# Performance work log

Measured on AMD Instinct MI355X. Metric: run time of the kernel, lower is better.

The kernel has to match this reference:

```python
import jax, jax.numpy as jnp
import numpy as np

N = 100000   # entities
T = 4        # edge types
E = 250000   # edges per type
D = 64       # dimension
H = 4        # attention heads
C = 64       # per-head out channels (PyG out_channels)
F_IN = 256   # raw feature dim
L = 2        # num_layers
NEG_SLOPE = 0.2


def setup_inputs() -> dict:
    key = jax.random.key(0)
    ks = jax.random.split(key, 10)
    return {
        "feature_matrix": jax.random.normal(ks[0], (N, F_IN), jnp.float32),
        "entity_emb": jax.random.normal(ks[1], (N + 1, D), jnp.float32),
        "lin_w": jax.random.normal(ks[2], (F_IN, D), jnp.float32) * 0.05,
        "lin_b": jnp.zeros((D,), jnp.float32),
        "ln_g": jnp.ones((D,), jnp.float32),
        "ln_b": jnp.zeros((D,), jnp.float32),
        "W_src": jax.random.normal(ks[3], (L, T, D, H * C), jnp.float32) * 0.1,
        "W_dst": jax.random.normal(ks[4], (L, T, D, H * C), jnp.float32) * 0.1,
        "a_src": jax.random.normal(ks[5], (L, T, H, C), jnp.float32) * 0.1,
        "a_dst": jax.random.normal(ks[6], (L, T, H, C), jnp.float32) * 0.1,
        "conv_bias": jnp.zeros((L, T, C), jnp.float32),
        "edge_index": jax.random.randint(ks[7], (T, 2, E), 0, N, jnp.int32),
    }


def _layer_norm(x, g, b):
    mu = jnp.mean(x, axis=-1, keepdims=True)
    var = jnp.var(x, axis=-1, keepdims=True)
    return (x - mu) * jax.lax.rsqrt(var + 1e-5) * g + b


def _l2_normalize(x):
    n = jnp.linalg.norm(x, axis=-1, keepdims=True)
    return x / jnp.maximum(n, 1e-12)


def _gat_conv(x, src, dst, Ws, Wd, a_s, a_d, bias):
    # x: [N, D]; src/dst: [E'] (self loops already appended, PyG default)
    xs = (x @ Ws).reshape(N, H, C)          # source projection per head
    xd = (x @ Wd).reshape(N, H, C)          # destination projection per head
    logit = (xs * a_s).sum(-1)[src] + (xd * a_d).sum(-1)[dst]  # [E', H]
    logit = jax.nn.leaky_relu(logit, NEG_SLOPE)
    # segment softmax over incoming edges of each dst node
    m = jax.lax.stop_gradient(jax.ops.segment_max(logit, dst, num_segments=N))
    p = jnp.exp(logit - m[dst])
    s = jax.ops.segment_sum(p, dst, num_segments=N)
    alpha = p / s[dst]                       # [E', H]
    msg = xs[src] * alpha[..., None]         # [E', H, C]
    out = jax.ops.segment_sum(msg.reshape(-1, H * C), dst, num_segments=N)
    out = out.reshape(N, H, C).mean(axis=1)  # concat=False -> head mean
    return out + bias


def reference(feature_matrix, entity_emb, lin_w, lin_b, ln_g, ln_b,
              W_src, W_dst, a_src, a_dst, conv_bias, edge_index):
    # feature_transform: Linear -> LayerNorm -> GELU (exact erf GELU, torch default)
    xf = jax.nn.gelu(_layer_norm(feature_matrix @ lin_w + lin_b, ln_g, ln_b),
                     approximate=False)
    xe = _l2_normalize(entity_emb[:N])
    x = xf + xe
    loop = jnp.arange(N, dtype=edge_index.dtype)
    for l in range(L):
        acc = jnp.zeros((N, C), x.dtype)
        for t in range(T):
            src = jnp.concatenate([edge_index[t, 0], loop])
            dst = jnp.concatenate([edge_index[t, 1], loop])
            acc = acc + _gat_conv(x, src, dst, W_src[l, t], W_dst[l, t],
                                  a_src[l, t], a_dst[l, t], conv_bias[l, t])
        x = jax.nn.gelu(acc / T, approximate=False)  # HeteroConv aggr='mean'; dropout=eval identity
    return x
```

## Files before the change

### kernel.cpp

```cpp
#include <hip/hip_runtime.h>
#include <hip/hip_bf16.h>
#include <cstdint>

#define NN   100000
#define TT   4
#define EE   250000
#define LL   2
#define NCH  49
#define EPN  (EE + NN)
#define N64  ((size_t)NN * 64)

typedef unsigned short ushort_t;
typedef __attribute__((ext_vector_type(8))) short bf16x8;
typedef __attribute__((ext_vector_type(16))) float floatx16;

static __device__ __forceinline__ float gelu_exact(float v) {
    return 0.5f * v * (1.0f + erff(v * 0.7071067811865476f));
}
static __device__ __forceinline__ float wave_sum64(float v) {
    #pragma unroll
    for (int m = 32; m; m >>= 1) v += __shfl_xor(v, m, 64);
    return v;
}
static __device__ __forceinline__ ushort_t f2bf(float f) {
    unsigned u = __float_as_uint(f);
    u += 0x7FFFu + ((u >> 16) & 1u);
    return (ushort_t)(u >> 16);
}
static __device__ __forceinline__ float bf2f(ushort_t h) {
    return __uint_as_float((unsigned)h << 16);
}
static __device__ __forceinline__ void gl_lds16(const ushort_t* g, ushort_t* l) {
    __builtin_amdgcn_global_load_lds(
        (const __attribute__((address_space(1))) void*)g,
        (__attribute__((address_space(3))) void*)l, 16, 0, 0);
}

__global__ __launch_bounds__(256) void k_prep(
    const float* __restrict__ Wsrc, const float* __restrict__ Wdst,
    const float* __restrict__ asrc, const float* __restrict__ adst,
    const float* __restrict__ cb, const float* __restrict__ lin_w,
    ushort_t* __restrict__ wcTh, ushort_t* __restrict__ wcTl,
    ushort_t* __restrict__ lwTh, ushort_t* __restrict__ lwTl,
    ushort_t* __restrict__ bpTh, ushort_t* __restrict__ bpTl,
    float* __restrict__ bsum)
{
    int id = blockIdx.x * 256 + threadIdx.x;
    {
        int d = id & 63;
        int c = (id >> 6) & 63;
        int h = (id >> 12) & 3;
        int t = (id >> 14) & 3;
        int l = (id >> 16) & 1;
        float v = 0.25f * Wsrc[(((l * 4 + t) * 64 + d) * 256) + h * 64 + c];
        int dst = (l * 64 + c) * 1024 + (t * 256 + h * 64 + d);
        ushort_t hh = f2bf(v);
        bpTh[dst] = hh;
        bpTl[dst] = f2bf(v - bf2f(hh));
    }
    if (id < LL * 64 * 64) {
        int d   = id & 63;
        int col = (id >> 6) & 63;
        int l   = (id >> 12) & 1;
        int t = col >> 3, side = (col >> 2) & 1, h = col & 3;
        const float* W = side ? Wdst : Wsrc;
        const float* a = side ? adst : asrc;
        int wb = ((l * 4 + t) * 64 + d) * 256 + h * 64;
        int ab = ((l * 4 + t) * 4 + h) * 64;
        float s = 0.f;
        #pragma unroll 8
        for (int c2 = 0; c2 < 64; ++c2) s = fmaf(W[wb + c2], a[ab + c2], s);
        int dst = (l * 64 + col) * 64 + d;
        ushort_t hh = f2bf(s);
        wcTh[dst] = hh;
        wcTl[dst] = f2bf(s - bf2f(hh));
    }
    if (id < 64 * 256) {
        int k = id & 255, c = id >> 8;
        float v = lin_w[k * 64 + c];
        ushort_t hh = f2bf(v);
        lwTh[c * 256 + k] = hh;
        lwTl[c * 256 + k] = f2bf(v - bf2f(hh));
    }
    if (id < LL * 64) {
        int l = id >> 6, c = id & 63;
        float s = 0.f;
        for (int t = 0; t < TT; ++t) s += cb[(l * 4 + t) * 64 + c];
        bsum[id] = s;
    }
}

__global__ void k_hist(const int* __restrict__ ei, int* __restrict__ cursor) {
    int id = blockIdx.x * 256 + threadIdx.x;
    if (id >= TT * EE) return;
    int t = id / EE, e = id - t * EE;
    int d = ei[(t * 2 + 1) * EE + e];
    atomicAdd(&cursor[t * NN + d], 1);
}

__global__ __launch_bounds__(256) void k_scan1(const int* __restrict__ deg,
                                               int* __restrict__ csum) {
    int b = blockIdx.x, t = b / NCH, cc = b - t * NCH;
    int tid = threadIdx.x;
    int base = cc * 2048 + tid * 8;
    int s = 0;
    #pragma unroll
    for (int i = 0; i < 8; ++i) {
        int idx = base + i;
        if (idx < NN) s += deg[t * NN + idx] + 1;
    }
    #pragma unroll
    for (int m = 32; m; m >>= 1) s += __shfl_xor(s, m, 64);
    __shared__ int ws4[4];
    int lane = tid & 63, wid = tid >> 6;
    if (lane == 0) ws4[wid] = s;
    __syncthreads();
    if (tid == 0) csum[b] = ws4[0] + ws4[1] + ws4[2] + ws4[3];
}

__global__ void k_scan2(const int* __restrict__ csum, int* __restrict__ cbase,
                        int* __restrict__ row_ptr) {
    int t = threadIdx.x;
    if (t >= TT) return;
    int base = 0;
    for (int c = 0; c < NCH; ++c) {
        cbase[t * NCH + c] = base;
        base += csum[t * NCH + c];
    }
    row_ptr[t * (NN + 1) + NN] = base;
}

__global__ __launch_bounds__(256) void k_scan3(int* __restrict__ cursor,
                                               const int* __restrict__ cbase,
                                               int* __restrict__ row_ptr) {
    int b = blockIdx.x, t = b / NCH, cc = b - t * NCH;
    int tid = threadIdx.x, lane = tid & 63, wid = tid >> 6;
    int base = cc * 2048 + tid * 8;
    int vals[8], ts = 0;
    #pragma unroll
    for (int i = 0; i < 8; ++i) {
        int idx = base + i;
        int v = (idx < NN) ? cursor[t * NN + idx] + 1 : 0;
        vals[i] = v; ts += v;
    }
    int v = ts;
    #pragma unroll
    for (int off = 1; off < 64; off <<= 1) {
        int u = __shfl_up(v, off, 64);
        if (lane >= off) v += u;
    }
    __shared__ int wt[4];
    if (lane == 63) wt[wid] = v;
    __syncthreads();
    int wbase = 0;
    for (int w = 0; w < wid; ++w) wbase += wt[w];
    int run = cbase[t * NCH + cc] + wbase + (v - ts);
    #pragma unroll
    for (int i = 0; i < 8; ++i) {
        int idx = base + i;
        if (idx < NN) {
            row_ptr[t * (NN + 1) + idx] = run;
            cursor[t * NN + idx] = run;
        }
        run += vals[i];
    }
}

__global__ void k_scatter(const int* __restrict__ ei, int* __restrict__ cursor,
                          int2* __restrict__ sd) {
    int id = blockIdx.x * 256 + threadIdx.x;
    if (id >= TT * EPN) return;
    int t = id / EPN, r = id - t * EPN;
    int s, d;
    if (r < EE) { s = ei[t * 2 * EE + r]; d = ei[(t * 2 + 1) * EE + r]; }
    else        { s = d = r - EE; }
    int pos = atomicAdd(&cursor[t * NN + d], 1);
    sd[(size_t)t * EPN + pos] = make_int2(s, d);
}

template <int FLAGS>
__global__ __launch_bounds__(256, 4) void k_gemm_mx(
    const ushort_t* __restrict__ Ahi, const ushort_t* __restrict__ Alo,
    const ushort_t* __restrict__ Bhi, const ushort_t* __restrict__ Blo,
    int K, int ldb, int nrows,
    const float* __restrict__ accbuf, const float* __restrict__ bias,
    float* __restrict__ Cout)
{
    constexpr int KC = 32;
    __shared__ ushort_t sAh[128 * 32], sAl[128 * 32];
    __shared__ ushort_t sBh[64 * 32],  sBl[64 * 32];
    const int tid = threadIdx.x;
    const int w = tid >> 6, ln = tid & 63;
    const int l31 = ln & 31, hl = ln >> 5;
    const int rowbase = blockIdx.x * 128;

    floatx16 accv[2];
    #pragma unroll
    for (int ct = 0; ct < 2; ++ct)
        #pragma unroll
        for (int r = 0; r < 16; ++r) accv[ct][r] = 0.f;

    for (int kc = 0; kc < K; kc += KC) {
        __syncthreads();
        #pragma unroll
        for (int i = 0; i < 2; ++i) {
            int f = tid + i * 256;
            int r = f >> 2, cg = f & 3;
            int row = rowbase + r;
            int sg = (r ^ (r >> 2)) & 3;
            if constexpr (FLAGS & 8) {
                int sw = r * 32 + ((cg ^ sg) << 3);
                if (row < nrows) {
                    const float* Af = (const float*)Ahi;
                    size_t ga = (size_t)row * K + kc + cg * 8;
                    float4 v0 = *(const float4*)(Af + ga);
                    float4 v1 = *(const float4*)(Af + ga + 4);
                    float vf[8] = {v0.x, v0.y, v0.z, v0.w, v1.x, v1.y, v1.z, v1.w};
                    unsigned hu[8], lu[8];
                    #pragma unroll
                    for (int q = 0; q < 8; ++q) {
                        ushort_t hh = f2bf(vf[q]);
                        hu[q] = hh;
                        lu[q] = f2bf(vf[q] - bf2f(hh));
                    }
                    uint4 H = make_uint4(hu[0] | (hu[1] << 16), hu[2] | (hu[3] << 16),
                                         hu[4] | (hu[5] << 16), hu[6] | (hu[7] << 16));
                    uint4 L = make_uint4(lu[0] | (lu[1] << 16), lu[2] | (lu[3] << 16),
                                         lu[4] | (lu[5] << 16), lu[6] | (lu[7] << 16));
                    *(uint4*)&sAh[sw] = H;
                    *(uint4*)&sAl[sw] = L;
                } else {
                    *(uint4*)&sAh[sw] = make_uint4(0, 0, 0, 0);
                    *(uint4*)&sAl[sw] = make_uint4(0, 0, 0, 0);
                }
            } else {
                int so = r * 32 + (cg << 3);
                size_t ga = (size_t)row * K + kc + ((cg ^ sg) << 3);
                if (row < nrows) {
                    gl_lds16(Ahi + ga, &sAh[so]);
                    gl_lds16(Alo + ga, &sAl[so]);
                }
            }
        }
        {
            int r = tid >> 2, cg = tid & 3;
            int sg = (r ^ (r >> 2)) & 3;
            int so = r * 32 + (cg << 3);
            size_t gb = (size_t)r * ldb + kc + ((cg ^ sg) << 3);
            gl_lds16(Bhi + gb, &sBh[so]);
            gl_lds16(Blo + gb, &sBl[so]);
        }
        __syncthreads();
        const int arow = (w << 5) + l31;
        const int sga = (arow ^ (arow >> 2)) & 3;
        const int sgb = (l31 ^ (l31 >> 2)) & 3;
        #pragma unroll
        for (int s = 0; s < 2; ++s) {
            const int c0 = (s << 1) | hl;
            const int ka = (c0 ^ sga) << 3;
            const int kb = (c0 ^ sgb) << 3;
            bf16x8 ah  = *(const bf16x8*)&sAh[arow * 32 + ka];
            bf16x8 al  = *(const bf16x8*)&sAl[arow * 32 + ka];
            bf16x8 bh0 = *(const bf16x8*)&sBh[l31 * 32 + kb];
            bf16x8 bl0 = *(const bf16x8*)&sBl[l31 * 32 + kb];
            bf16x8 bh1 = *(const bf16x8*)&sBh[(32 + l31) * 32 + kb];
            bf16x8 bl1 = *(const bf16x8*)&sBl[(32 + l31) * 32 + kb];
            accv[0] = __builtin_amdgcn_mfma_f32_32x32x16_bf16(ah, bh0, accv[0], 0, 0, 0);
            accv[1] = __builtin_amdgcn_mfma_f32_32x32x16_bf16(ah, bh1, accv[1], 0, 0, 0);
            accv[0] = __builtin_amdgcn_mfma_f32_32x32x16_bf16(al, bh0, accv[0], 0, 0, 0);
            accv[1] = __builtin_amdgcn_mfma_f32_32x32x16_bf16(al, bh1, accv[1], 0, 0, 0);
            accv[0] = __builtin_amdgcn_mfma_f32_32x32x16_bf16(ah, bl0, accv[0], 0, 0, 0);
            accv[1] = __builtin_amdgcn_mfma_f32_32x32x16_bf16(ah, bl1, accv[1], 0, 0, 0);
        }
    }
    #pragma unroll
    for (int ct = 0; ct < 2; ++ct) {
        int col = (ct << 5) + l31;
        float bv = (FLAGS & 2) ? bias[col] : 0.f;
        #pragma unroll
        for (int r = 0; r < 16; ++r) {
            int row = rowbase + (w << 5) + (r & 3) + ((r >> 2) << 3) + (hl << 2);
            if (row < nrows) {
                size_t idx = (size_t)row * 64 + col;
                float v = accv[ct][r];
                if (FLAGS & 1) v += accbuf[idx];
                if (FLAGS & 2) v = gelu_exact((v + bv) * 0.25f);
                Cout[idx] = v;
            }
        }
    }
}

__global__ __launch_bounds__(256) void k_feat_post(
    const float* __restrict__ y, const float* __restrict__ lin_b,
    const float* __restrict__ ln_g, const float* __restrict__ ln_b,
    const float* __restrict__ emb, float* __restrict__ xout)
{
    int n = (blockIdx.x << 2) + (threadIdx.x >> 6);
    int c = threadIdx.x & 63;
    size_t base = (size_t)n * 64 + c;
    float v = y[base] + lin_b[c];
    float mean = wave_sum64(v) * 0.015625f;
    float t = v - mean;
    float var = wave_sum64(t * t) * 0.015625f;
    float vn = t * (1.0f / sqrtf(var + 1e-5f)) * ln_g[c] + ln_b[c];
    float g = gelu_exact(vn);
    float e = emb[base];
    float nrm = sqrtf(wave_sum64(e * e));
    float xv = g + e / fmaxf(nrm, 1e-12f);
    xout[base] = xv;
}

__global__ __launch_bounds__(256) void k_edgep(
    const float* __restrict__ s_all, const int2* __restrict__ sd,
    float* __restrict__ parr)
{
    int i = blockIdx.x * 256 + threadIdx.x;
    int t = blockIdx.y;
    if (i >= EPN) return;
    size_t base = (size_t)t * EPN + i;
    int2 e = sd[base];
    const float4 a = *(const float4*)&s_all[(size_t)e.x * 64 + t * 8];
    const float4 b = *(const float4*)&s_all[(size_t)e.y * 64 + t * 8 + 4];
    float l0 = a.x + b.x, l1 = a.y + b.y;
    float l2 = a.z + b.z, l3 = a.w + b.w;
    l0 = l0 > 0.f ? l0 : 0.2f * l0;
    l1 = l1 > 0.f ? l1 : 0.2f * l1;
    l2 = l2 > 0.f ? l2 : 0.2f * l2;
    l3 = l3 > 0.f ? l3 : 0.2f * l3;
    float4 p = make_float4(__expf(l0), __expf(l1), __expf(l2), __expf(l3));
    *(float4*)&parr[base * 4] = p;
}

__global__ __launch_bounds__(256) void k_edge2(
    const float* __restrict__ x, const float* __restrict__ parr,
    const int* __restrict__ row_ptr, const int2* __restrict__ sd,
    ushort_t* __restrict__ zh, ushort_t* __restrict__ zl, int t0)
{
    int n = (blockIdx.x << 2) + (threadIdx.x >> 6);
    int lane = threadIdx.x & 63;
    const int tA = t0, tB = t0 + 1;
    int eA  = row_ptr[tA * (NN + 1) + n];
    int eA1 = row_ptr[tA * (NN + 1) + n + 1];
    int eB  = row_ptr[tB * (NN + 1) + n];
    int eB1 = row_ptr[tB * (NN + 1) + n + 1];
    const int2*   sdA = sd + (size_t)tA * EPN;
    const float4* pA  = (const float4*)parr + (size_t)tA * EPN;
    const int2*   sdB = sd + (size_t)tB * EPN;
    const float4* pB  = (const float4*)parr + (size_t)tB * EPN;
    float a0 = 0.f, a1 = 0.f, a2 = 0.f, a3 = 0.f;
    float SA0 = 0.f, SA1 = 0.f, SA2 = 0.f, SA3 = 0.f;
    float b0 = 0.f, b1 = 0.f, b2 = 0.f, b3 = 0.f;
    float SB0 = 0.f, SB1 = 0.f, SB2 = 0.f, SB3 = 0.f;
    int m = (eA1 - eA < eB1 - eB) ? (eA1 - eA) : (eB1 - eB);
    #pragma unroll 2
    for (int i = 0; i < m; ++i) {
        int sA_ = sdA[eA + i].x;
        int sB_ = sdB[eB + i].x;
        float4 pa = pA[eA + i];
        float4 pb = pB[eB + i];
        float xa = x[(size_t)sA_ * 64 + lane];
        float xb = x[(size_t)sB_ * 64 + lane];
        SA0 += pa.x; SA1 += pa.y; SA2 += pa.z; SA3 += pa.w;
        SB0 += pb.x; SB1 += pb.y; SB2 += pb.z; SB3 += pb.w;
        a0 = fmaf(pa.x, xa, a0); a1 = fmaf(pa.y, xa, a1);
        a2 = fmaf(pa.z, xa, a2); a3 = fmaf(pa.w, xa, a3);
        b0 = fmaf(pb.x, xb, b0); b1 = fmaf(pb.y, xb, b1);
        b2 = fmaf(pb.z, xb, b2); b3 = fmaf(pb.w, xb, b3);
    }
    eA += m; eB += m;
    for (; eA < eA1; ++eA) {
        int s = sdA[eA].x; float4 p = pA[eA];
        float xv = x[(size_t)s * 64 + lane];
        SA0 += p.x; SA1 += p.y; SA2 += p.z; SA3 += p.w;
        a0 = fmaf(p.x, xv, a0); a1 = fmaf(p.y, xv, a1);
        a2 = fmaf(p.z, xv, a2); a3 = fmaf(p.w, xv, a3);
    }
    for (; eB < eB1; ++eB) {
        int s = sdB[eB].x; float4 p = pB[eB];
        float xv = x[(size_t)s * 64 + lane];
        SB0 += p.x; SB1 += p.y; SB2 += p.z; SB3 += p.w;
        b0 = fmaf(p.x, xv, b0); b1 = fmaf(p.y, xv, b1);
        b2 = fmaf(p.z, xv, b2); b3 = fmaf(p.w, xv, b3);
    }
    size_t zb = (size_t)n * 512 + lane;
    {
        float v0 = a0 / SA0, v1 = a1 / SA1, v2 = a2 / SA2, v3 = a3 / SA3;
        ushort_t h0 = f2bf(v0), h1 = f2bf(v1), h2 = f2bf(v2), h3 = f2bf(v3);
        zh[zb]       = h0;  zl[zb]       = f2bf(v0 - bf2f(h0));
        zh[zb + 64]  = h1;  zl[zb + 64]  = f2bf(v1 - bf2f(h1));
        zh[zb + 128] = h2;  zl[zb + 128] = f2bf(v2 - bf2f(h2));
        zh[zb + 192] = h3;  zl[zb + 192] = f2bf(v3 - bf2f(h3));
    }
    {
        size_t zc = zb + 256;
        float v0 = b0 / SB0, v1 = b1 / SB1, v2 = b2 / SB2, v3 = b3 / SB3;
        ushort_t h0 = f2bf(v0), h1 = f2bf(v1), h2 = f2bf(v2), h3 = f2bf(v3);
        zh[zc]       = h0;  zl[zc]       = f2bf(v0 - bf2f(h0));
        zh[zc + 64]  = h1;  zl[zc + 64]  = f2bf(v1 - bf2f(h1));
        zh[zc + 128] = h2;  zl[zc + 128] = f2bf(v2 - bf2f(h2));
        zh[zc + 192] = h3;  zl[zc + 192] = f2bf(v3 - bf2f(h3));
    }
}

extern "C" void kernel_launch(void* const* d_in, const int* in_sizes, int n_in,
                              void* d_out, int out_size, void* d_ws, size_t ws_size,
                              hipStream_t stream) {
    const float* fm    = (const float*)d_in[0];
    const float* emb   = (const float*)d_in[1];
    const float* lin_w = (const float*)d_in[2];
    const float* lin_b = (const float*)d_in[3];
    const float* ln_g  = (const float*)d_in[4];
    const float* ln_b  = (const float*)d_in[5];
    const float* Wsrc  = (const float*)d_in[6];
    const float* Wdst  = (const float*)d_in[7];
    const float* asrc  = (const float*)d_in[8];
    const float* adst  = (const float*)d_in[9];
    const float* cbias = (const float*)d_in[10];
    const int*   ei    = (const int*)d_in[11];
    float* out = (float*)d_out;
    (void)in_sizes; (void)n_in; (void)out_size; (void)ws_size;

    char* w = (char*)d_ws;
    size_t off = 0;
    auto alloc = [&](size_t bytes) -> void* {
        void* p = w + off;
        off += (bytes + 255) & ~(size_t)255;
        return p;
    };
    ushort_t* wcTh = (ushort_t*)alloc((size_t)LL * 64 * 64 * 2);
    ushort_t* wcTl = (ushort_t*)alloc((size_t)LL * 64 * 64 * 2);
    ushort_t* lwTh = (ushort_t*)alloc((size_t)64 * 256 * 2);
    ushort_t* lwTl = (ushort_t*)alloc((size_t)64 * 256 * 2);
    ushort_t* bpTh = (ushort_t*)alloc((size_t)LL * 64 * 1024 * 2);
    ushort_t* bpTl = (ushort_t*)alloc((size_t)LL * 64 * 1024 * 2);
    float* bsum    = (float*)alloc((size_t)LL * 64 * 4);
    int*   row_ptr = (int*)  alloc((size_t)TT * (NN + 1) * 4);
    int*   cursor  = (int*)  alloc((size_t)TT * NN * 4);
    int2*  sdarr   = (int2*) alloc((size_t)TT * EPN * 8);
    float* parr    = (float*)alloc((size_t)TT * EPN * 4 * 4);
    int*   csum    = (int*)  alloc((size_t)TT * NCH * 4);
    int*   cbase   = (int*)  alloc((size_t)TT * NCH * 4);
    float* x       = (float*)alloc(N64 * 4);
    float* s_all   = (float*)alloc(N64 * 4);
    float* accB    = (float*)alloc(N64 * 4);
    size_t planeE = (size_t)NN * 512;
    ushort_t* zh = (ushort_t*)alloc(2 * planeE * 2);
    ushort_t* zl = zh + planeE;

    hipMemsetAsync(cursor, 0, (size_t)TT * NN * 4, stream);
    k_prep<<<512, 256, 0, stream>>>(Wsrc, Wdst, asrc, adst, cbias, lin_w,
                                    wcTh, wcTl, lwTh, lwTl, bpTh, bpTl, bsum);
    k_hist<<<(TT * EE + 255) / 256, 256, 0, stream>>>(ei, cursor);
    k_scan1<<<TT * NCH, 256, 0, stream>>>(cursor, csum);
    k_scan2<<<1, 64, 0, stream>>>(csum, cbase, row_ptr);
    k_scan3<<<TT * NCH, 256, 0, stream>>>(cursor, cbase, row_ptr);
    k_scatter<<<(TT * EPN + 255) / 256, 256, 0, stream>>>(ei, cursor, sdarr);

    const int GB = (NN + 127) / 128;
    k_gemm_mx<8><<<GB, 256, 0, stream>>>((const ushort_t*)fm, nullptr,
                                         lwTh, lwTl, 256, 256, NN,
                                         nullptr, nullptr, accB);
    k_feat_post<<<NN / 4, 256, 0, stream>>>(accB, lin_b, ln_g, ln_b, emb, x);

    const dim3 gp((EPN + 255) / 256, TT);
    for (int l = 0; l < LL; ++l) {
        float* dest = (l == 0) ? x : out;
        k_gemm_mx<8><<<GB, 256, 0, stream>>>((const ushort_t*)x, nullptr,
                                             wcTh + l * 4096, wcTl + l * 4096,
                                             64, 64, NN, nullptr, nullptr, s_all);
        k_edgep<<<gp, 256, 0, stream>>>(s_all, sdarr, parr);
        const ushort_t* Bh = bpTh + (size_t)l * 65536;
        const ushort_t* Bl = bpTl + (size_t)l * 65536;
        k_edge2<<<NN / 4, 256, 0, stream>>>(x, parr, row_ptr, sdarr, zh, zl, 0);
        k_gemm_mx<0><<<GB, 256, 0, stream>>>(zh, zl, Bh, Bl, 512, 1024, NN,
                                             nullptr, nullptr, accB);
        k_edge2<<<NN / 4, 256, 0, stream>>>(x, parr, row_ptr, sdarr, zh, zl, 2);
        k_gemm_mx<3><<<GB, 256, 0, stream>>>(zh, zl, Bh + 512, Bl + 512, 512, 1024,
                                             NN, accB, bsum + l * 64, dest);
    }
}
```

Measured before the change: 1.024 ms.

## Fuse edge aggregation with projection GEMM via shared-memory bf16 staging

Replaces the two edge-aggregation kernels and two split bf16 GEMMs per layer with one fused kernel. Each block aggregates attention-weighted neighbor features for 64 nodes per edge type into LDS as hi/lo bf16, then multiplies by the per-type projection with MFMA, and applies bias plus GELU at the end. This removes the large z intermediate (N×512 hi/lo planes) written to and read back from global memory, and uses ping-pong x buffers. The cost is lower occupancy from about 64KB of LDS per block and serialization between the gather phase and the MFMA phase within a block.

```diff
diff --git a/kernel.cpp b/kernel.cpp
--- a/kernel.cpp
+++ b/kernel.cpp
@@ -13,6 +13,7 @@
 typedef unsigned short ushort_t;
 typedef __attribute__((ext_vector_type(8))) short bf16x8;
 typedef __attribute__((ext_vector_type(16))) float floatx16;
+typedef __attribute__((ext_vector_type(4))) float floatx4;
 
 static __device__ __forceinline__ float gelu_exact(float v) {
     return 0.5f * v * (1.0f + erff(v * 0.7071067811865476f));
@@ -53,7 +54,7 @@
         int t = (id >> 14) & 3;
         int l = (id >> 16) & 1;
         float v = 0.25f * Wsrc[(((l * 4 + t) * 64 + d) * 256) + h * 64 + c];
-        int dst = (l * 64 + c) * 1024 + (t * 256 + h * 64 + d);
+        int dst = (l * 64 + c) * 1024 + (t * 256 + d * 4 + h);
         ushort_t hh = f2bf(v);
         bpTh[dst] = hh;
         bpTl[dst] = f2bf(v - bf2f(hh));
@@ -178,13 +179,10 @@
     sd[(size_t)t * EPN + pos] = make_int2(s, d);
 }
 
-template <int FLAGS>
-__global__ __launch_bounds__(256, 4) void k_gemm_mx(
-    const ushort_t* __restrict__ Ahi, const ushort_t* __restrict__ Alo,
+__global__ __launch_bounds__(256, 4) void k_gemm_f32a(
+    const float* __restrict__ Af,
     const ushort_t* __restrict__ Bhi, const ushort_t* __restrict__ Blo,
-    int K, int ldb, int nrows,
-    const float* __restrict__ accbuf, const float* __restrict__ bias,
-    float* __restrict__ Cout)
+    int K, int ldb, int nrows, float* __restrict__ Cout)
 {
     constexpr int KC = 32;
     __shared__ ushort_t sAh[128 * 32], sAl[128 * 32];
@@ -208,38 +206,28 @@
             int r = f >> 2, cg = f & 3;
             int row = rowbase + r;
             int sg = (r ^ (r >> 2)) & 3;
-            if constexpr (FLAGS & 8) {
-                int sw = r * 32 + ((cg ^ sg) << 3);
-                if (row < nrows) {
-                    const float* Af = (const float*)Ahi;
-                    size_t ga = (size_t)row * K + kc + cg * 8;
-                    float4 v0 = *(const float4*)(Af + ga);
-                    float4 v1 = *(const float4*)(Af + ga + 4);
-                    float vf[8] = {v0.x, v0.y, v0.z, v0.w, v1.x, v1.y, v1.z, v1.w};
-                    unsigned hu[8], lu[8];
-                    #pragma unroll
-                    for (int q = 0; q < 8; ++q) {
-                        ushort_t hh = f2bf(vf[q]);
-                        hu[q] = hh;
-                        lu[q] = f2bf(vf[q] - bf2f(hh));
-                    }
-                    uint4 H = make_uint4(hu[0] | (hu[1] << 16), hu[2] | (hu[3] << 16),
-                                         hu[4] | (hu[5] << 16), hu[6] | (hu[7] << 16));
-                    uint4 L = make_uint4(lu[0] | (lu[1] << 16), lu[2] | (lu[3] << 16),
-                                         lu[4] | (lu[5] << 16), lu[6] | (lu[7] << 16));
-                    *(uint4*)&sAh[sw] = H;
-                    *(uint4*)&sAl[sw] = L;
-                } else {
-                    *(uint4*)&sAh[sw] = make_uint4(0, 0, 0, 0);
-                    *(uint4*)&sAl[sw] = make_uint4(0, 0, 0, 0);
+            int sw = r * 32 + ((cg ^ sg) << 3);
+            if (row < nrows) {
+                size_t ga = (size_t)row * K + kc + cg * 8;
+                floatx4 v0 = *(const floatx4*)(Af + ga);
+                floatx4 v1 = *(const floatx4*)(Af + ga + 4);
+                float vf[8] = {v0.x, v0.y, v0.z, v0.w, v1.x, v1.y, v1.z, v1.w};
+                unsigned hu[8], lu[8];
+                #pragma unroll
+                for (int q = 0; q < 8; ++q) {
+                    ushort_t hh = f2bf(vf[q]);
+                    hu[q] = hh;
+                    lu[q] = f2bf(vf[q] - bf2f(hh));
                 }
+                uint4 H = make_uint4(hu[0] | (hu[1] << 16), hu[2] | (hu[3] << 16),
+                                     hu[4] | (hu[5] << 16), hu[6] | (hu[7] << 16));
+                uint4 L = make_uint4(lu[0] | (lu[1] << 16), lu[2] | (lu[3] << 16),
+                                     lu[4] | (lu[5] << 16), lu[6] | (lu[7] << 16));
+                *(uint4*)&sAh[sw] = H;
+                *(uint4*)&sAl[sw] = L;
             } else {
-                int so = r * 32 + (cg << 3);
-                size_t ga = (size_t)row * K + kc + ((cg ^ sg) << 3);
-                if (row < nrows) {
-                    gl_lds16(Ahi + ga, &sAh[so]);
-                    gl_lds16(Alo + ga, &sAl[so]);
-                }
+                *(uint4*)&sAh[sw] = make_uint4(0, 0, 0, 0);
+                *(uint4*)&sAl[sw] = make_uint4(0, 0, 0, 0);
             }
         }
         {
@@ -276,17 +264,10 @@
     #pragma unroll
     for (int ct = 0; ct < 2; ++ct) {
         int col = (ct << 5) + l31;
-        float bv = (FLAGS & 2) ? bias[col] : 0.f;
         #pragma unroll
         for (int r = 0; r < 16; ++r) {
             int row = rowbase + (w << 5) + (r & 3) + ((r >> 2) << 3) + (hl << 2);
-            if (row < nrows) {
-                size_t idx = (size_t)row * 64 + col;
-                float v = accv[ct][r];
-                if (FLAGS & 1) v += accbuf[idx];
-                if (FLAGS & 2) v = gelu_exact((v + bv) * 0.25f);
-                Cout[idx] = v;
-            }
+            if (row < nrows) Cout[(size_t)row * 64 + col] = accv[ct][r];
         }
     }
 }
@@ -332,74 +313,137 @@
     *(float4*)&parr[base * 4] = p;
 }
 
-__global__ __launch_bounds__(256) void k_edge2(
+__global__ __launch_bounds__(256) void k_fused(
     const float* __restrict__ x, const float* __restrict__ parr,
     const int* __restrict__ row_ptr, const int2* __restrict__ sd,
-    ushort_t* __restrict__ zh, ushort_t* __restrict__ zl, int t0)
+    const ushort_t* __restrict__ Bh, const ushort_t* __restrict__ Bl,
+    const float* __restrict__ bias, float* __restrict__ dest)
 {
-    int n = (blockIdx.x << 2) + (threadIdx.x >> 6);
-    int lane = threadIdx.x & 63;
-    const int tA = t0, tB = t0 + 1;
-    int eA  = row_ptr[tA * (NN + 1) + n];
-    int eA1 = row_ptr[tA * (NN + 1) + n + 1];
-    int eB  = row_ptr[tB * (NN + 1) + n];
-    int eB1 = row_ptr[tB * (NN + 1) + n + 1];
-    const int2*   sdA = sd + (size_t)tA * EPN;
-    const float4* pA  = (const float4*)parr + (size_t)tA * EPN;
-    const int2*   sdB = sd + (size_t)tB * EPN;
-    const float4* pB  = (const float4*)parr + (size_t)tB * EPN;
-    float a0 = 0.f, a1 = 0.f, a2 = 0.f, a3 = 0.f;
-    float SA0 = 0.f, SA1 = 0.f, SA2 = 0.f, SA3 = 0.f;
-    float b0 = 0.f, b1 = 0.f, b2 = 0.f, b3 = 0.f;
-    float SB0 = 0.f, SB1 = 0.f, SB2 = 0.f, SB3 = 0.f;
-    int m = (eA1 - eA < eB1 - eB) ? (eA1 - eA) : (eB1 - eB);
-    #pragma unroll 2
-    for (int i = 0; i < m; ++i) {
-        int sA_ = sdA[eA + i].x;
-        int sB_ = sdB[eB + i].x;
-        float4 pa = pA[eA + i];
-        float4 pb = pB[eB + i];
-        float xa = x[(size_t)sA_ * 64 + lane];
-        float xb = x[(size_t)sB_ * 64 + lane];
-        SA0 += pa.x; SA1 += pa.y; SA2 += pa.z; SA3 += pa.w;
-        SB0 += pb.x; SB1 += pb.y; SB2 += pb.z; SB3 += pb.w;
-        a0 = fmaf(pa.x, xa, a0); a1 = fmaf(pa.y, xa, a1);
-        a2 = fmaf(pa.z, xa, a2); a3 = fmaf(pa.w, xa, a3);
-        b0 = fmaf(pb.x, xb, b0); b1 = fmaf(pb.y, xb, b1);
-        b2 = fmaf(pb.z, xb, b2); b3 = fmaf(pb.w, xb, b3);
-    }
-    eA += m; eB += m;
-    for (; eA < eA1; ++eA) {
-        int s = sdA[eA].x; float4 p = pA[eA];
-        float xv = x[(size_t)s * 64 + lane];
-        SA0 += p.x; SA1 += p.y; SA2 += p.z; SA3 += p.w;
-        a0 = fmaf(p.x, xv, a0); a1 = fmaf(p.y, xv, a1);
-        a2 = fmaf(p.z, xv, a2); a3 = fmaf(p.w, xv, a3);
-    }
-    for (; eB < eB1; ++eB) {
-        int s = sdB[eB].x; float4 p = pB[eB];
-        float xv = x[(size_t)s * 64 + lane];
-        SB0 += p.x; SB1 += p.y; SB2 += p.z; SB3 += p.w;
-        b0 = fmaf(p.x, xv, b0); b1 = fmaf(p.y, xv, b1);
-        b2 = fmaf(p.z, xv, b2); b3 = fmaf(p.w, xv, b3);
-    }
-    size_t zb = (size_t)n * 512 + lane;
-    {
-        float v0 = a0 / SA0, v1 = a1 / SA1, v2 = a2 / SA2, v3 = a3 / SA3;
-        ushort_t h0 = f2bf(v0), h1 = f2bf(v1), h2 = f2bf(v2), h3 = f2bf(v3);
-        zh[zb]       = h0;  zl[zb]       = f2bf(v0 - bf2f(h0));
-        zh[zb + 64]  = h1;  zl[zb + 64]  = f2bf(v1 - bf2f(h1));
-        zh[zb + 128] = h2;  zl[zb + 128] = f2bf(v2 - bf2f(h2));
-        zh[zb + 192] = h3;  zl[zb + 192] = f2bf(v3 - bf2f(h3));
-    }
-    {
-        size_t zc = zb + 256;
-        float v0 = b0 / SB0, v1 = b1 / SB1, v2 = b2 / SB2, v3 = b3 / SB3;
-        ushort_t h0 = f2bf(v0), h1 = f2bf(v1), h2 = f2bf(v2), h3 = f2bf(v3);
-        zh[zc]       = h0;  zl[zc]       = f2bf(v0 - bf2f(h0));
-        zh[zc + 64]  = h1;  zl[zc + 64]  = f2bf(v1 - bf2f(h1));
-        zh[zc + 128] = h2;  zl[zc + 128] = f2bf(v2 - bf2f(h2));
-        zh[zc + 192] = h3;  zl[zc + 192] = f2bf(v3 - bf2f(h3));
+    __shared__ ushort_t zH[64 * 256], zL[64 * 256];
+    __shared__ ushort_t sBh[64 * 32], sBl[64 * 32];
+    const int tid = threadIdx.x;
+    const int w = tid >> 6, lane = tid & 63;
+    const int l31 = lane & 31, hl = lane >> 5;
+    const int rt = w >> 1, ct = w & 1;
+    const int rowbase = blockIdx.x * 64;
+
+    floatx16 acc;
+    #pragma unroll
+    for (int r = 0; r < 16; ++r) acc[r] = 0.f;
+
+    for (int t = 0; t < TT; ++t) {
+        const int*     srcs = (const int*)(sd + (size_t)t * EPN);
+        const floatx4* pt   = (const floatx4*)parr + (size_t)t * EPN;
+        const int* rp = row_ptr + t * (NN + 1);
+        #pragma unroll 1
+        for (int i = 0; i < 8; ++i) {
+            int lrA = (w << 4) + i, lrB = lrA + 8;
+            int nA = rowbase + lrA, nB = rowbase + lrB;
+            float a0 = 0.f, a1 = 0.f, a2 = 0.f, a3 = 0.f;
+            float SA0 = 0.f, SA1 = 0.f, SA2 = 0.f, SA3 = 0.f;
+            float b0 = 0.f, b1 = 0.f, b2 = 0.f, b3 = 0.f;
+            float SB0 = 0.f, SB1 = 0.f, SB2 = 0.f, SB3 = 0.f;
+            int eA = 0, eA1 = 0, eB = 0, eB1 = 0;
+            if (nA < NN) { eA = rp[nA]; eA1 = rp[nA + 1]; }
+            if (nB < NN) { eB = rp[nB]; eB1 = rp[nB + 1]; }
+            int m = (eA1 - eA < eB1 - eB) ? (eA1 - eA) : (eB1 - eB);
+            #pragma unroll 2
+            for (int q = 0; q < m; ++q) {
+                int sA_ = srcs[2 * (eA + q)];
+                int sB_ = srcs[2 * (eB + q)];
+                floatx4 pa = pt[eA + q];
+                floatx4 pb = pt[eB + q];
+                float xa = x[(size_t)sA_ * 64 + lane];
+                float xb = x[(size_t)sB_ * 64 + lane];
+                SA0 += pa.x; SA1 += pa.y; SA2 += pa.z; SA3 += pa.w;
+                SB0 += pb.x; SB1 += pb.y; SB2 += pb.z; SB3 += pb.w;
+                a0 = fmaf(pa.x, xa, a0); a1 = fmaf(pa.y, xa, a1);
+                a2 = fmaf(pa.z, xa, a2); a3 = fmaf(pa.w, xa, a3);
+                b0 = fmaf(pb.x, xb, b0); b1 = fmaf(pb.y, xb, b1);
+                b2 = fmaf(pb.z, xb, b2); b3 = fmaf(pb.w, xb, b3);
+            }
+            eA += m; eB += m;
+            for (; eA < eA1; ++eA) {
+                int s = srcs[2 * eA]; floatx4 p = pt[eA];
+                float xv = x[(size_t)s * 64 + lane];
+                SA0 += p.x; SA1 += p.y; SA2 += p.z; SA3 += p.w;
+                a0 = fmaf(p.x, xv, a0); a1 = fmaf(p.y, xv, a1);
+                a2 = fmaf(p.z, xv, a2); a3 = fmaf(p.w, xv, a3);
+            }
+            for (; eB < eB1; ++eB) {
+                int s = srcs[2 * eB]; floatx4 p = pt[eB];
+                float xv = x[(size_t)s * 64 + lane];
+                SB0 += p.x; SB1 += p.y; SB2 += p.z; SB3 += p.w;
+                b0 = fmaf(p.x, xv, b0); b1 = fmaf(p.y, xv, b1);
+                b2 = fmaf(p.z, xv, b2); b3 = fmaf(p.w, xv, b3);
+            }
+            int gsw = ((lane >> 1) ^ (lrA & 31)) << 3;
+            int go = lrA * 256 + gsw + ((lane & 1) << 2);
+            {
+                float v0 = (nA < NN) ? a0 / SA0 : 0.f;
+                float v1 = (nA < NN) ? a1 / SA1 : 0.f;
+                float v2 = (nA < NN) ? a2 / SA2 : 0.f;
+                float v3 = (nA < NN) ? a3 / SA3 : 0.f;
+                unsigned h0 = f2bf(v0), h1 = f2bf(v1), h2 = f2bf(v2), h3 = f2bf(v3);
+                *(uint2*)&zH[go] = make_uint2(h0 | (h1 << 16), h2 | (h3 << 16));
+                unsigned l0 = f2bf(v0 - bf2f((ushort_t)h0));
+                unsigned l1 = f2bf(v1 - bf2f((ushort_t)h1));
+                unsigned l2 = f2bf(v2 - bf2f((ushort_t)h2));
+                unsigned l3 = f2bf(v3 - bf2f((ushort_t)h3));
+                *(uint2*)&zL[go] = make_uint2(l0 | (l1 << 16), l2 | (l3 << 16));
+            }
+            int gswB = ((lane >> 1) ^ (lrB & 31)) << 3;
+            int goB = lrB * 256 + gswB + ((lane & 1) << 2);
+            {
+                float v0 = (nB < NN) ? b0 / SB0 : 0.f;
+                float v1 = (nB < NN) ? b1 / SB1 : 0.f;
+                float v2 = (nB < NN) ? b2 / SB2 : 0.f;
+                float v3 = (nB < NN) ? b3 / SB3 : 0.f;
+                unsigned h0 = f2bf(v0), h1 = f2bf(v1), h2 = f2bf(v2), h3 = f2bf(v3);
+                *(uint2*)&zH[goB] = make_uint2(h0 | (h1 << 16), h2 | (h3 << 16));
+                unsigned l0 = f2bf(v0 - bf2f((ushort_t)h0));
+                unsigned l1 = f2bf(v1 - bf2f((ushort_t)h1));
+                unsigned l2 = f2bf(v2 - bf2f((ushort_t)h2));
+                unsigned l3 = f2bf(v3 - bf2f((ushort_t)h3));
+                *(uint2*)&zL[goB] = make_uint2(l0 | (l1 << 16), l2 | (l3 << 16));
+            }
+        }
+        __syncthreads();
+        const int am = (rt << 5) + l31;
+        const int brow = (ct << 5) + l31;
+        const int sgb = (l31 ^ (l31 >> 2)) & 3;
+        for (int kc = 0; kc < 8; ++kc) {
+            {
+                int r = tid >> 2, cg = tid & 3;
+                int sg = (r ^ (r >> 2)) & 3;
+                size_t gb = (size_t)r * 1024 + t * 256 + kc * 32 + ((cg ^ sg) << 3);
+                gl_lds16(Bh + gb, &sBh[r * 32 + cg * 8]);
+                gl_lds16(Bl + gb, &sBl[r * 32 + cg * 8]);
+            }
+            __syncthreads();
+            #pragma unroll
+            for (int s = 0; s < 2; ++s) {
+                int gg = kc * 4 + (s << 1) + hl;
+                int ao = am * 256 + ((gg ^ (am & 31)) << 3);
+                bf16x8 ah = *(const bf16x8*)&zH[ao];
+                bf16x8 al = *(const bf16x8*)&zL[ao];
+                int kb = (((s << 1) | hl) ^ sgb) << 3;
+                bf16x8 bh = *(const bf16x8*)&sBh[brow * 32 + kb];
+                bf16x8 bl = *(const bf16x8*)&sBl[brow * 32 + kb];
+                acc = __builtin_amdgcn_mfma_f32_32x32x16_bf16(ah, bh, acc, 0, 0, 0);
+                acc = __builtin_amdgcn_mfma_f32_32x32x16_bf16(al, bh, acc, 0, 0, 0);
+                acc = __builtin_amdgcn_mfma_f32_32x32x16_bf16(ah, bl, acc, 0, 0, 0);
+            }
+            __syncthreads();
+        }
+    }
+    int col = (ct << 5) + l31;
+    float bv = bias[col];
+    #pragma unroll
+    for (int r = 0; r < 16; ++r) {
+        int row = rowbase + (rt << 5) + (r & 3) + ((r >> 2) << 3) + (hl << 2);
+        if (row < NN)
+            dest[(size_t)row * 64 + col] = gelu_exact((acc[r] + bv) * 0.25f);
     }
 }
 
@@ -442,11 +486,9 @@
     int*   csum    = (int*)  alloc((size_t)TT * NCH * 4);
     int*   cbase   = (int*)  alloc((size_t)TT * NCH * 4);
     float* x       = (float*)alloc(N64 * 4);
+    float* xnew    = (float*)alloc(N64 * 4);
     float* s_all   = (float*)alloc(N64 * 4);
-    float* accB    = (float*)alloc(N64 * 4);
-    size_t planeE = (size_t)NN * 512;
-    ushort_t* zh = (ushort_t*)alloc(2 * planeE * 2);
-    ushort_t* zl = zh + planeE;
+    float* ybuf    = (float*)alloc(N64 * 4);
 
     hipMemsetAsync(cursor, 0, (size_t)TT * NN * 4, stream);
     k_prep<<<512, 256, 0, stream>>>(Wsrc, Wdst, asrc, adst, cbias, lin_w,
@@ -458,25 +500,20 @@
     k_scatter<<<(TT * EPN + 255) / 256, 256, 0, stream>>>(ei, cursor, sdarr);
 
     const int GB = (NN + 127) / 128;
-    k_gemm_mx<8><<<GB, 256, 0, stream>>>((const ushort_t*)fm, nullptr,
-                                         lwTh, lwTl, 256, 256, NN,
-                                         nullptr, nullptr, accB);
-    k_feat_post<<<NN / 4, 256, 0, stream>>>(accB, lin_b, ln_g, ln_b, emb, x);
+    k_gemm_f32a<<<GB, 256, 0, stream>>>(fm, lwTh, lwTl, 256, 256, NN, ybuf);
+    k_feat_post<<<NN / 4, 256, 0, stream>>>(ybuf, lin_b, ln_g, ln_b, emb, x);
 
     const dim3 gp((EPN + 255) / 256, TT);
+    const int FB = (NN + 63) / 64;
     for (int l = 0; l < LL; ++l) {
-        float* dest = (l == 0) ? x : out;
-        k_gemm_mx<8><<<GB, 256, 0, stream>>>((const ushort_t*)x, nullptr,
-                                             wcTh + l * 4096, wcTl + l * 4096,
-                                             64, 64, NN, nullptr, nullptr, s_all);
+        const float* xin = (l == 0) ? x : xnew;
+        float* dest = (l == 0) ? xnew : out;
+        k_gemm_f32a<<<GB, 256, 0, stream>>>(xin, wcTh + l * 4096, wcTl + l * 4096,
+                                            64, 64, NN, s_all);
         k_edgep<<<gp, 256, 0, stream>>>(s_all, sdarr, parr);
-        const ushort_t* Bh = bpTh + (size_t)l * 65536;
-        const ushort_t* Bl = bpTl + (size_t)l * 65536;
-        k_edge2<<<NN / 4, 256, 0, stream>>>(x, parr, row_ptr, sdarr, zh, zl, 0);
-        k_gemm_mx<0><<<GB, 256, 0, stream>>>(zh, zl, Bh, Bl, 512, 1024, NN,
-                                             nullptr, nullptr, accB);
-        k_edge2<<<NN / 4, 256, 0, stream>>>(x, parr, row_ptr, sdarr, zh, zl, 2);
-        k_gemm_mx<3><<<GB, 256, 0, stream>>>(zh, zl, Bh + 512, Bl + 512, 512, 1024,
-                                             NN, accB, bsum + l * 64, dest);
-    }
-}
+        k_fused<<<FB, 256, 0, stream>>>(xin, parr, row_ptr, sdarr,
+                                        bpTh + (size_t)l * 65536,
+                                        bpTl + (size_t)l * 65536,
+                                        bsum + l * 64, dest);
+    }
+}
```

New measurement: 1.225 ms. +19.7%, slower.

## Handle self-loops inline and split GEMM into f32-input and 64-row variants

Applied to the files above, without the earlier changes.

Self-loop edges are no longer materialised in the CSR, scatter and edge-parameter arrays. Instead each node's self-loop logit is computed directly from s_all inside k_edge2 and used to seed the softmax sum and the accumulators. The GEMM is split into a 128-row kernel for the fp32-input projections and a new 64-row-tile k_gemm64 for the K=512 aggregation GEMMs. The smaller tile launches more blocks and requests higher occupancy. This cuts edge-array traffic and the number of scatter atomics, but adds per-node exp work and changes the tile shape of the large GEMMs.

```diff
diff --git a/kernel.cpp b/kernel.cpp
--- a/kernel.cpp
+++ b/kernel.cpp
@@ -7,12 +7,12 @@
 #define EE   250000
 #define LL   2
 #define NCH  49
-#define EPN  (EE + NN)
 #define N64  ((size_t)NN * 64)
 
 typedef unsigned short ushort_t;
 typedef __attribute__((ext_vector_type(8))) short bf16x8;
 typedef __attribute__((ext_vector_type(16))) float floatx16;
+typedef __attribute__((ext_vector_type(4))) float floatx4;
 
 static __device__ __forceinline__ float gelu_exact(float v) {
     return 0.5f * v * (1.0f + erff(v * 0.7071067811865476f));
@@ -107,7 +107,7 @@
     #pragma unroll
     for (int i = 0; i < 8; ++i) {
         int idx = base + i;
-        if (idx < NN) s += deg[t * NN + idx] + 1;
+        if (idx < NN) s += deg[t * NN + idx];
     }
     #pragma unroll
     for (int m = 32; m; m >>= 1) s += __shfl_xor(s, m, 64);
@@ -140,7 +140,7 @@
     #pragma unroll
     for (int i = 0; i < 8; ++i) {
         int idx = base + i;
-        int v = (idx < NN) ? cursor[t * NN + idx] + 1 : 0;
+        int v = (idx < NN) ? cursor[t * NN + idx] : 0;
         vals[i] = v; ts += v;
     }
     int v = ts;
@@ -169,22 +169,18 @@
 __global__ void k_scatter(const int* __restrict__ ei, int* __restrict__ cursor,
                           int2* __restrict__ sd) {
     int id = blockIdx.x * 256 + threadIdx.x;
-    if (id >= TT * EPN) return;
-    int t = id / EPN, r = id - t * EPN;
-    int s, d;
-    if (r < EE) { s = ei[t * 2 * EE + r]; d = ei[(t * 2 + 1) * EE + r]; }
-    else        { s = d = r - EE; }
+    if (id >= TT * EE) return;
+    int t = id / EE, r = id - t * EE;
+    int s = ei[t * 2 * EE + r];
+    int d = ei[(t * 2 + 1) * EE + r];
     int pos = atomicAdd(&cursor[t * NN + d], 1);
-    sd[(size_t)t * EPN + pos] = make_int2(s, d);
-}
-
-template <int FLAGS>
-__global__ __launch_bounds__(256, 4) void k_gemm_mx(
-    const ushort_t* __restrict__ Ahi, const ushort_t* __restrict__ Alo,
+    sd[(size_t)t * EE + pos] = make_int2(s, d);
+}
+
+__global__ __launch_bounds__(256, 4) void k_gemm_f32a(
+    const float* __restrict__ Af,
     const ushort_t* __restrict__ Bhi, const ushort_t* __restrict__ Blo,
-    int K, int ldb, int nrows,
-    const float* __restrict__ accbuf, const float* __restrict__ bias,
-    float* __restrict__ Cout)
+    int K, int ldb, int nrows, float* __restrict__ Cout)
 {
     constexpr int KC = 32;
     __shared__ ushort_t sAh[128 * 32], sAl[128 * 32];
@@ -208,38 +204,28 @@
             int r = f >> 2, cg = f & 3;
             int row = rowbase + r;
             int sg = (r ^ (r >> 2)) & 3;
-            if constexpr (FLAGS & 8) {
-                int sw = r * 32 + ((cg ^ sg) << 3);
-                if (row < nrows) {
-                    const float* Af = (const float*)Ahi;
-                    size_t ga = (size_t)row * K + kc + cg * 8;
-                    float4 v0 = *(const float4*)(Af + ga);
-                    float4 v1 = *(const float4*)(Af + ga + 4);
-                    float vf[8] = {v0.x, v0.y, v0.z, v0.w, v1.x, v1.y, v1.z, v1.w};
-                    unsigned hu[8], lu[8];
-                    #pragma unroll
-                    for (int q = 0; q < 8; ++q) {
-                        ushort_t hh = f2bf(vf[q]);
-                        hu[q] = hh;
-                        lu[q] = f2bf(vf[q] - bf2f(hh));
-                    }
-                    uint4 H = make_uint4(hu[0] | (hu[1] << 16), hu[2] | (hu[3] << 16),
-                                         hu[4] | (hu[5] << 16), hu[6] | (hu[7] << 16));
-                    uint4 L = make_uint4(lu[0] | (lu[1] << 16), lu[2] | (lu[3] << 16),
-                                         lu[4] | (lu[5] << 16), lu[6] | (lu[7] << 16));
-                    *(uint4*)&sAh[sw] = H;
-                    *(uint4*)&sAl[sw] = L;
-                } else {
-                    *(uint4*)&sAh[sw] = make_uint4(0, 0, 0, 0);
-                    *(uint4*)&sAl[sw] = make_uint4(0, 0, 0, 0);
+            int sw = r * 32 + ((cg ^ sg) << 3);
+            if (row < nrows) {
+                size_t ga = (size_t)row * K + kc + cg * 8;
+                floatx4 v0 = *(const floatx4*)(Af + ga);
+                floatx4 v1 = *(const floatx4*)(Af + ga + 4);
+                float vf[8] = {v0.x, v0.y, v0.z, v0.w, v1.x, v1.y, v1.z, v1.w};
+                unsigned hu[8], lu[8];
+                #pragma unroll
+                for (int q = 0; q < 8; ++q) {
+                    ushort_t hh = f2bf(vf[q]);
+                    hu[q] = hh;
+                    lu[q] = f2bf(vf[q] - bf2f(hh));
                 }
+                uint4 H = make_uint4(hu[0] | (hu[1] << 16), hu[2] | (hu[3] << 16),
+                                     hu[4] | (hu[5] << 16), hu[6] | (hu[7] << 16));
+                uint4 L = make_uint4(lu[0] | (lu[1] << 16), lu[2] | (lu[3] << 16),
+                                     lu[4] | (lu[5] << 16), lu[6] | (lu[7] << 16));
+                *(uint4*)&sAh[sw] = H;
+                *(uint4*)&sAl[sw] = L;
             } else {
-                int so = r * 32 + (cg << 3);
-                size_t ga = (size_t)row * K + kc + ((cg ^ sg) << 3);
-                if (row < nrows) {
-                    gl_lds16(Ahi + ga, &sAh[so]);
-                    gl_lds16(Alo + ga, &sAl[so]);
-                }
+                *(uint4*)&sAh[sw] = make_uint4(0, 0, 0, 0);
+                *(uint4*)&sAl[sw] = make_uint4(0, 0, 0, 0);
             }
         }
         {
@@ -276,17 +262,81 @@
     #pragma unroll
     for (int ct = 0; ct < 2; ++ct) {
         int col = (ct << 5) + l31;
-        float bv = (FLAGS & 2) ? bias[col] : 0.f;
         #pragma unroll
         for (int r = 0; r < 16; ++r) {
             int row = rowbase + (w << 5) + (r & 3) + ((r >> 2) << 3) + (hl << 2);
+            if (row < nrows) Cout[(size_t)row * 64 + col] = accv[ct][r];
+        }
+    }
+}
+
+template <int FLAGS>
+__global__ __launch_bounds__(256, 6) void k_gemm64(
+    const ushort_t* __restrict__ Ahi, const ushort_t* __restrict__ Alo,
+    const ushort_t* __restrict__ Bhi, const ushort_t* __restrict__ Blo,
+    int K, int ldb, int nrows,
+    const float* __restrict__ accbuf, const float* __restrict__ bias,
+    float* __restrict__ Cout)
+{
+    constexpr int KC = 32;
+    __shared__ ushort_t sAh[64 * 32], sAl[64 * 32];
+    __shared__ ushort_t sBh[64 * 32], sBl[64 * 32];
+    const int tid = threadIdx.x;
+    const int w = tid >> 6, ln = tid & 63;
+    const int l31 = ln & 31, hl = ln >> 5;
+    const int rt = w >> 1, ct = w & 1;
+    const int rowbase = blockIdx.x * 64;
+
+    floatx16 acc;
+    #pragma unroll
+    for (int r = 0; r < 16; ++r) acc[r] = 0.f;
+
+    for (int kc = 0; kc < K; kc += KC) {
+        __syncthreads();
+        {
+            int r = tid >> 2, cg = tid & 3;
+            int sg = (r ^ (r >> 2)) & 3;
+            int so = r * 32 + (cg << 3);
+            int row = rowbase + r;
             if (row < nrows) {
-                size_t idx = (size_t)row * 64 + col;
-                float v = accv[ct][r];
-                if (FLAGS & 1) v += accbuf[idx];
-                if (FLAGS & 2) v = gelu_exact((v + bv) * 0.25f);
-                Cout[idx] = v;
+                size_t ga = (size_t)row * K + kc + ((cg ^ sg) << 3);
+                gl_lds16(Ahi + ga, &sAh[so]);
+                gl_lds16(Alo + ga, &sAl[so]);
             }
+            size_t gb = (size_t)r * ldb + kc + ((cg ^ sg) << 3);
+            gl_lds16(Bhi + gb, &sBh[so]);
+            gl_lds16(Blo + gb, &sBl[so]);
+        }
+        __syncthreads();
+        const int arow = (rt << 5) + l31;
+        const int brow = (ct << 5) + l31;
+        const int sga = (arow ^ (arow >> 2)) & 3;
+        const int sgb = (l31 ^ (l31 >> 2)) & 3;
+        #pragma unroll
+        for (int s = 0; s < 2; ++s) {
+            const int c0 = (s << 1) | hl;
+            const int ka = (c0 ^ sga) << 3;
+            const int kb = (c0 ^ sgb) << 3;
+            bf16x8 ah = *(const bf16x8*)&sAh[arow * 32 + ka];
+            bf16x8 al = *(const bf16x8*)&sAl[arow * 32 + ka];
+            bf16x8 bh = *(const bf16x8*)&sBh[brow * 32 + kb];
+            bf16x8 bl = *(const bf16x8*)&sBl[brow * 32 + kb];
+            acc = __builtin_amdgcn_mfma_f32_32x32x16_bf16(ah, bh, acc, 0, 0, 0);
+            acc = __builtin_amdgcn_mfma_f32_32x32x16_bf16(al, bh, acc, 0, 0, 0);
+            acc = __builtin_amdgcn_mfma_f32_32x32x16_bf16(ah, bl, acc, 0, 0, 0);
+        }
+    }
+    int col = (ct << 5) + l31;
+    float bv = (FLAGS & 2) ? bias[col] : 0.f;
+    #pragma unroll
+    for (int r = 0; r < 16; ++r) {
+        int row = rowbase + (rt << 5) + (r & 3) + ((r >> 2) << 3) + (hl << 2);
+        if (row < nrows) {
+            size_t idx = (size_t)row * 64 + col;
+            float v = acc[r];
+            if (FLAGS & 1) v += accbuf[idx];
+            if (FLAGS & 2) v = gelu_exact((v + bv) * 0.25f);
+            Cout[idx] = v;
         }
     }
 }
@@ -317,8 +367,8 @@
 {
     int i = blockIdx.x * 256 + threadIdx.x;
     int t = blockIdx.y;
-    if (i >= EPN) return;
-    size_t base = (size_t)t * EPN + i;
+    if (i >= EE) return;
+    size_t base = (size_t)t * EE + i;
     int2 e = sd[base];
     const float4 a = *(const float4*)&s_all[(size_t)e.x * 64 + t * 8];
     const float4 b = *(const float4*)&s_all[(size_t)e.y * 64 + t * 8 + 4];
@@ -333,8 +383,9 @@
 }
 
 __global__ __launch_bounds__(256) void k_edge2(
-    const float* __restrict__ x, const float* __restrict__ parr,
-    const int* __restrict__ row_ptr, const int2* __restrict__ sd,
+    const float* __restrict__ x, const float* __restrict__ s_all,
+    const float* __restrict__ parr, const int* __restrict__ row_ptr,
+    const int2* __restrict__ sd,
     ushort_t* __restrict__ zh, ushort_t* __restrict__ zl, int t0)
 {
     int n = (blockIdx.x << 2) + (threadIdx.x >> 6);
@@ -344,21 +395,40 @@
     int eA1 = row_ptr[tA * (NN + 1) + n + 1];
     int eB  = row_ptr[tB * (NN + 1) + n];
     int eB1 = row_ptr[tB * (NN + 1) + n + 1];
-    const int2*   sdA = sd + (size_t)tA * EPN;
-    const float4* pA  = (const float4*)parr + (size_t)tA * EPN;
-    const int2*   sdB = sd + (size_t)tB * EPN;
-    const float4* pB  = (const float4*)parr + (size_t)tB * EPN;
-    float a0 = 0.f, a1 = 0.f, a2 = 0.f, a3 = 0.f;
-    float SA0 = 0.f, SA1 = 0.f, SA2 = 0.f, SA3 = 0.f;
-    float b0 = 0.f, b1 = 0.f, b2 = 0.f, b3 = 0.f;
-    float SB0 = 0.f, SB1 = 0.f, SB2 = 0.f, SB3 = 0.f;
+    const int*     sA = (const int*)(sd + (size_t)tA * EE);
+    const floatx4* pA = (const floatx4*)parr + (size_t)tA * EE;
+    const int*     sB = (const int*)(sd + (size_t)tB * EE);
+    const floatx4* pB = (const floatx4*)parr + (size_t)tB * EE;
+    float xn = x[(size_t)n * 64 + lane];
+    float a0, a1, a2, a3, SA0, SA1, SA2, SA3;
+    float b0, b1, b2, b3, SB0, SB1, SB2, SB3;
+    {
+        const float4 sa = *(const float4*)&s_all[(size_t)n * 64 + tA * 8];
+        const float4 sb = *(const float4*)&s_all[(size_t)n * 64 + tA * 8 + 4];
+        float l0 = sa.x + sb.x, l1 = sa.y + sb.y;
+        float l2 = sa.z + sb.z, l3 = sa.w + sb.w;
+        l0 = l0 > 0.f ? l0 : 0.2f * l0;  l1 = l1 > 0.f ? l1 : 0.2f * l1;
+        l2 = l2 > 0.f ? l2 : 0.2f * l2;  l3 = l3 > 0.f ? l3 : 0.2f * l3;
+        SA0 = __expf(l0); SA1 = __expf(l1); SA2 = __expf(l2); SA3 = __expf(l3);
+        a0 = SA0 * xn; a1 = SA1 * xn; a2 = SA2 * xn; a3 = SA3 * xn;
+    }
+    {
+        const float4 sa = *(const float4*)&s_all[(size_t)n * 64 + tB * 8];
+        const float4 sb = *(const float4*)&s_all[(size_t)n * 64 + tB * 8 + 4];
+        float l0 = sa.x + sb.x, l1 = sa.y + sb.y;
+        float l2 = sa.z + sb.z, l3 = sa.w + sb.w;
+        l0 = l0 > 0.f ? l0 : 0.2f * l0;  l1 = l1 > 0.f ? l1 : 0.2f * l1;
+        l2 = l2 > 0.f ? l2 : 0.2f * l2;  l3 = l3 > 0.f ? l3 : 0.2f * l3;
+        SB0 = __expf(l0); SB1 = __expf(l1); SB2 = __expf(l2); SB3 = __expf(l3);
+        b0 = SB0 * xn; b1 = SB1 * xn; b2 = SB2 * xn; b3 = SB3 * xn;
+    }
     int m = (eA1 - eA < eB1 - eB) ? (eA1 - eA) : (eB1 - eB);
     #pragma unroll 2
     for (int i = 0; i < m; ++i) {
-        int sA_ = sdA[eA + i].x;
-        int sB_ = sdB[eB + i].x;
-        float4 pa = pA[eA + i];
-        float4 pb = pB[eB + i];
+        int sA_ = sA[2 * (eA + i)];
+        int sB_ = sB[2 * (eB + i)];
+        floatx4 pa = pA[eA + i];
+        floatx4 pb = pB[eB + i];
         float xa = x[(size_t)sA_ * 64 + lane];
         float xb = x[(size_t)sB_ * 64 + lane];
         SA0 += pa.x; SA1 += pa.y; SA2 += pa.z; SA3 += pa.w;
@@ -370,14 +440,14 @@
     }
     eA += m; eB += m;
     for (; eA < eA1; ++eA) {
-        int s = sdA[eA].x; float4 p = pA[eA];
+        int s = sA[2 * eA]; floatx4 p = pA[eA];
         float xv = x[(size_t)s * 64 + lane];
         SA0 += p.x; SA1 += p.y; SA2 += p.z; SA3 += p.w;
         a0 = fmaf(p.x, xv, a0); a1 = fmaf(p.y, xv, a1);
         a2 = fmaf(p.z, xv, a2); a3 = fmaf(p.w, xv, a3);
     }
     for (; eB < eB1; ++eB) {
-        int s = sdB[eB].x; float4 p = pB[eB];
+        int s = sB[2 * eB]; floatx4 p = pB[eB];
         float xv = x[(size_t)s * 64 + lane];
         SB0 += p.x; SB1 += p.y; SB2 += p.z; SB3 += p.w;
         b0 = fmaf(p.x, xv, b0); b1 = fmaf(p.y, xv, b1);
@@ -437,8 +507,8 @@
     float* bsum    = (float*)alloc((size_t)LL * 64 * 4);
     int*   row_ptr = (int*)  alloc((size_t)TT * (NN + 1) * 4);
     int*   cursor  = (int*)  alloc((size_t)TT * NN * 4);
-    int2*  sdarr   = (int2*) alloc((size_t)TT * EPN * 8);
-    float* parr    = (float*)alloc((size_t)TT * EPN * 4 * 4);
+    int2*  sdarr   = (int2*) alloc((size_t)TT * EE * 8);
+    float* parr    = (float*)alloc((size_t)TT * EE * 4 * 4);
     int*   csum    = (int*)  alloc((size_t)TT * NCH * 4);
     int*   cbase   = (int*)  alloc((size_t)TT * NCH * 4);
     float* x       = (float*)alloc(N64 * 4);
@@ -455,28 +525,28 @@
     k_scan1<<<TT * NCH, 256, 0, stream>>>(cursor, csum);
     k_scan2<<<1, 64, 0, stream>>>(csum, cbase, row_ptr);
     k_scan3<<<TT * NCH, 256, 0, stream>>>(cursor, cbase, row_ptr);
-    k_scatter<<<(TT * EPN + 255) / 256, 256, 0, stream>>>(ei, cursor, sdarr);
-
-    const int GB = (NN + 127) / 128;
-    k_gemm_mx<8><<<GB, 256, 0, stream>>>((const ushort_t*)fm, nullptr,
-                                         lwTh, lwTl, 256, 256, NN,
-                                         nullptr, nullptr, accB);
+    k_scatter<<<(TT * EE + 255) / 256, 256, 0, stream>>>(ei, cursor, sdarr);
+
+    const int GB  = (NN + 127) / 128;
+    const int GB2 = (NN + 63) / 64;
+    k_gemm_f32a<<<GB, 256, 0, stream>>>(fm, lwTh, lwTl, 256, 256, NN, accB);
     k_feat_post<<<NN / 4, 256, 0, stream>>>(accB, lin_b, ln_g, ln_b, emb, x);
 
-    const dim3 gp((EPN + 255) / 256, TT);
+    const dim3 gp((EE + 255) / 256, TT);
     for (int l = 0; l < LL; ++l) {
         float* dest = (l == 0) ? x : out;
-        k_gemm_mx<8><<<GB, 256, 0, stream>>>((const ushort_t*)x, nullptr,
-                                             wcTh + l * 4096, wcTl + l * 4096,
-                                             64, 64, NN, nullptr, nullptr, s_all);
+        k_gemm_f32a<<<GB, 256, 0, stream>>>(x, wcTh + l * 4096, wcTl + l * 4096,
+                                            64, 64, NN, s_all);
         k_edgep<<<gp, 256, 0, stream>>>(s_all, sdarr, parr);
         const ushort_t* Bh = bpTh + (size_t)l * 65536;
         const ushort_t* Bl = bpTl + (size_t)l * 65536;
-        k_edge2<<<NN / 4, 256, 0, stream>>>(x, parr, row_ptr, sdarr, zh, zl, 0);
-        k_gemm_mx<0><<<GB, 256, 0, stream>>>(zh, zl, Bh, Bl, 512, 1024, NN,
+        k_edge2<<<NN / 4, 256, 0, stream>>>(x, s_all, parr, row_ptr, sdarr,
+                                            zh, zl, 0);
+        k_gemm64<0><<<GB2, 256, 0, stream>>>(zh, zl, Bh, Bl, 512, 1024, NN,
                                              nullptr, nullptr, accB);
-        k_edge2<<<NN / 4, 256, 0, stream>>>(x, parr, row_ptr, sdarr, zh, zl, 2);
-        k_gemm_mx<3><<<GB, 256, 0, stream>>>(zh, zl, Bh + 512, Bl + 512, 512, 1024,
+        k_edge2<<<NN / 4, 256, 0, stream>>>(x, s_all, parr, row_ptr, sdarr,
+                                            zh, zl, 2);
+        k_gemm64<3><<<GB2, 256, 0, stream>>>(zh, zl, Bh + 512, Bl + 512, 512, 1024,
                                              NN, accB, bsum + l * 64, dest);
     }
 }
```

Result: no change. 1.019 ms (-0.5%).
